# Kernel optimization log

Measured on AMD Instinct MI355X. Metric: run time of the kernel, lower is better.

Reference implementation:

```python
import jax, jax.numpy as jnp
import numpy as np

D = 128
NH = 8
L = 3
DFF = 2048
DEPOT_IDX = 0
LN_EPS = 1e-5


def _ln(x, g, b):
    m = jnp.mean(x, -1, keepdims=True)
    v = jnp.mean((x - m) ** 2, -1, keepdims=True)
    return (x - m) / jnp.sqrt(v + LN_EPS) * g + b


def _mha(x, wqkv, bqkv, wo, bo):
    # torch nn.MultiheadAttention, batch_first, no dropout (eval)
    b, n, d = x.shape
    hd = d // NH
    qkv = x @ wqkv.T + bqkv                       # [b,n,3d]
    q, k, v = jnp.split(qkv, 3, axis=-1)
    sh = lambda t: t.reshape(b, n, NH, hd).transpose(0, 2, 1, 3)
    q, k, v = sh(q), sh(k), sh(v)
    att = jax.nn.softmax(jnp.einsum('bhqd,bhkd->bhqk', q, k) * (hd ** -0.5), axis=-1)
    o = jnp.einsum('bhqk,bhkd->bhqd', att, v).transpose(0, 2, 1, 3).reshape(b, n, d)
    return o @ wo.T + bo


def _encoder(c, w_inp, b_inp, wqkv, bqkv, wo, bo, w1, b1, w2, b2, g1, be1, g2, be2):
    h = c @ w_inp.T + b_inp                       # [b,n,d]

    def layer(h, p):
        (wqkv, bqkv, wo, bo, w1, b1, w2, b2, g1, be1, g2, be2) = p
        # post-LN TransformerEncoderLayer (torch default norm_first=False, relu)
        h = _ln(h + _mha(h, wqkv, bqkv, wo, bo), g1, be1)
        ff = jax.nn.relu(h @ w1.T + b1) @ w2.T + b2
        h = _ln(h + ff, g2, be2)
        return h, None

    h, _ = jax.lax.scan(layer, h, (wqkv, bqkv, wo, bo, w1, b1, w2, b2, g1, be1, g2, be2))
    return h


def _greedy(c, start_node, params):
    (w_inp, b_inp, wqkv, bqkv, wo, bo, w1, b1, w2, b2, g1, be1, g2, be2,
     wq, bq, wk, bk) = params
    b, n, _ = c.shape
    e = _encoder(c, w_inp, b_inp, wqkv, bqkv, wo, bo, w1, b1, w2, b2, g1, be1, g2, be2)
    kproj = e @ wk.T + bk                          # [b,n,d], hoisted (loop-invariant)
    scale = D ** (-0.5)
    neg = jnp.finfo(e.dtype).min
    bidx = jnp.arange(b)

    vis0 = jnp.zeros((b, n), bool).at[:, DEPOT_IDX].set(True)

    def step(carry, _):
        node, vis = carry
        mask = vis.at[bidx, node].set(True)
        q = e[bidx, node] @ wq.T + bq              # [b,d]
        logits = jnp.einsum('bd,bnd->bn', q, kproj) * scale
        logits = jnp.where(mask, neg, logits)
        nxt = jnp.argmax(logits, axis=-1)
        return (nxt, mask), (node, logits)

    (_, _), (tour, logits) = jax.lax.scan(step, (start_node, vis0), None, length=n - 1)
    return tour.T, logits.transpose(1, 0, 2)      # [b,n-1], [b,n-1,n]


def setup_inputs() -> dict:
    key = jax.random.key(0)
    ks = jax.random.split(key, 24)
    B, N = 512, 100
    w = lambda k, s: jax.random.normal(k, s, jnp.float32) * 0.05
    inp = {
        'c': jax.random.uniform(ks[0], (B, N, 2), jnp.float32),
        'start_node': jax.random.randint(ks[1], (B,), 1, N),
        'w_inp': w(ks[2], (D, 2)), 'b_inp': jnp.zeros((D,), jnp.float32),
        'wqkv': w(ks[3], (L, 3 * D, D)), 'bqkv': jnp.zeros((L, 3 * D), jnp.float32),
        'wo': w(ks[4], (L, D, D)), 'bo': jnp.zeros((L, D), jnp.float32),
        'w1': w(ks[5], (L, DFF, D)), 'b1': jnp.zeros((L, DFF), jnp.float32),
        'w2': w(ks[6], (L, D, DFF)), 'b2': jnp.zeros((L, D), jnp.float32),
        'g1': jnp.ones((L, D), jnp.float32), 'be1': jnp.zeros((L, D), jnp.float32),
        'g2': jnp.ones((L, D), jnp.float32), 'be2': jnp.zeros((L, D), jnp.float32),
        'wq': w(ks[7], (D, D)), 'bq': jnp.zeros((D,), jnp.float32),
        'wk': w(ks[8], (D, D)), 'bk': jnp.zeros((D,), jnp.float32),
    }
    return inp


def reference(c, start_node, w_inp, b_inp, wqkv, bqkv, wo, bo, w1, b1, w2, b2,
              g1, be1, g2, be2, wq, bq, wk, bk):
    params = (w_inp, b_inp, wqkv, bqkv, wo, bo, w1, b1, w2, b2,
              g1, be1, g2, be2, wq, bq, wk, bk)
    tour, logits = _greedy(c, start_node, params)
    return tour, logits
```

## Files before the change

kernel.cpp:

```cpp
#include <hip/hip_runtime.h>
#include <hip/hip_bf16.h>
#include <math.h>

#define D 128
#define NH 8
#define HD 16
#define NL 3
#define DFF 2048
#define NNODE 100
#define BATCH 512
#define M_TOT (BATCH * NNODE)
#define LN_EPS 1e-5f
#define NEGW (-3.0e+38f)

typedef __attribute__((ext_vector_type(8))) short bf16x8;
typedef __attribute__((ext_vector_type(4))) float f32x4;
typedef __attribute__((ext_vector_type(8))) unsigned short u16x8;

__device__ __forceinline__ unsigned short f2bf(float x) {
  unsigned u = __float_as_uint(x);
  u = u + 0x7FFFu + ((u >> 16) & 1u);
  return (unsigned short)(u >> 16);
}
__device__ __forceinline__ float bf2f(unsigned short s) {
  return __uint_as_float(((unsigned)s) << 16);
}

__global__ __launch_bounds__(256) void k_split(
    const float* __restrict__ src, unsigned short* __restrict__ hi,
    unsigned short* __restrict__ lo, int n) {
  int i = blockIdx.x * 256 + threadIdx.x;
  if (i >= n) return;
  float x = src[i];
  unsigned short h = f2bf(x);
  hi[i] = h;
  lo[i] = f2bf(x - bf2f(h));
}

__global__ __launch_bounds__(256) void k_inproj(
    const float* __restrict__ c, const float* __restrict__ w,
    const float* __restrict__ b, float* __restrict__ h,
    unsigned short* __restrict__ hhi, unsigned short* __restrict__ hlo) {
  int idx = blockIdx.x * 256 + threadIdx.x;
  if (idx >= M_TOT * D) return;
  int m = idx >> 7, d = idx & 127;
  float v = c[m * 2] * w[d * 2] + c[m * 2 + 1] * w[d * 2 + 1] + b[d];
  h[idx] = v;
  unsigned short t = f2bf(v);
  hhi[idx] = t;
  hlo[idx] = f2bf(v - bf2f(t));
}

__global__ __launch_bounds__(256) void k_gemm3(
    const unsigned short* __restrict__ Ah, const unsigned short* __restrict__ Al,
    const unsigned short* __restrict__ Wh, const unsigned short* __restrict__ Wl,
    const float* __restrict__ bias,
    float* __restrict__ C, unsigned short* __restrict__ Chi,
    unsigned short* __restrict__ Clo, int M, int N, int K, int relu_split) {
  __shared__ unsigned short sAh[64 * 40], sAl[64 * 40];
  __shared__ unsigned short sWh[128 * 40], sWl[128 * 40];
  const int m0 = blockIdx.x * 64, n0 = blockIdx.y * 128;
  const int tid = threadIdx.x, lane = tid & 63, wid = tid >> 6;
  const int wr = wid >> 1, wc = wid & 1;
  const int lr = lane & 15, lg = lane >> 4;
  f32x4 acc[2][4];
#pragma unroll
  for (int a = 0; a < 2; ++a)
#pragma unroll
    for (int b = 0; b < 4; ++b) acc[a][b] = (f32x4){0.f, 0.f, 0.f, 0.f};
  const int ar = tid >> 2, ak = (tid & 3) * 8;
  const int wrr = tid >> 1, wkk = (tid & 1) * 16;
  const bool a_ok = (m0 + ar) < M;
  const long long a_base = (long long)(m0 + ar) * K + ak;
  const long long w_base = (long long)(n0 + wrr) * K + wkk;
  for (int k0 = 0; k0 < K; k0 += 32) {
    u16x8 vah = {0, 0, 0, 0, 0, 0, 0, 0}, val = {0, 0, 0, 0, 0, 0, 0, 0};
    if (a_ok) {
      vah = *(const u16x8*)(Ah + a_base + k0);
      val = *(const u16x8*)(Al + a_base + k0);
    }
    u16x8 vwh0 = *(const u16x8*)(Wh + w_base + k0);
    u16x8 vwh1 = *(const u16x8*)(Wh + w_base + k0 + 8);
    u16x8 vwl0 = *(const u16x8*)(Wl + w_base + k0);
    u16x8 vwl1 = *(const u16x8*)(Wl + w_base + k0 + 8);
    __syncthreads();
    *(u16x8*)&sAh[ar * 40 + ak] = vah;
    *(u16x8*)&sAl[ar * 40 + ak] = val;
    *(u16x8*)&sWh[wrr * 40 + wkk] = vwh0;
    *(u16x8*)&sWh[wrr * 40 + wkk + 8] = vwh1;
    *(u16x8*)&sWl[wrr * 40 + wkk] = vwl0;
    *(u16x8*)&sWl[wrr * 40 + wkk + 8] = vwl1;
    __syncthreads();
    bf16x8 fah[2], fal[2], fwh[4], fwl[4];
#pragma unroll
    for (int fm = 0; fm < 2; ++fm) {
      int o = (wr * 32 + fm * 16 + lr) * 40 + lg * 8;
      fah[fm] = *(const bf16x8*)&sAh[o];
      fal[fm] = *(const bf16x8*)&sAl[o];
    }
#pragma unroll
    for (int fn = 0; fn < 4; ++fn) {
      int o = (wc * 64 + fn * 16 + lr) * 40 + lg * 8;
      fwh[fn] = *(const bf16x8*)&sWh[o];
      fwl[fn] = *(const bf16x8*)&sWl[o];
    }
#pragma unroll
    for (int fm = 0; fm < 2; ++fm)
#pragma unroll
      for (int fn = 0; fn < 4; ++fn) {
        acc[fm][fn] = __builtin_amdgcn_mfma_f32_16x16x32_bf16(
            fah[fm], fwl[fn], acc[fm][fn], 0, 0, 0);
        acc[fm][fn] = __builtin_amdgcn_mfma_f32_16x16x32_bf16(
            fal[fm], fwh[fn], acc[fm][fn], 0, 0, 0);
        acc[fm][fn] = __builtin_amdgcn_mfma_f32_16x16x32_bf16(
            fah[fm], fwh[fn], acc[fm][fn], 0, 0, 0);
      }
  }
#pragma unroll
  for (int fm = 0; fm < 2; ++fm) {
    int rb = m0 + wr * 32 + fm * 16 + lg * 4;
#pragma unroll
    for (int fn = 0; fn < 4; ++fn) {
      int col = n0 + wc * 64 + fn * 16 + lr;
      float bv = bias[col];
#pragma unroll
      for (int j = 0; j < 4; ++j) {
        int row = rb + j;
        if (row < M) {
          float v = acc[fm][fn][j] + bv;
          if (relu_split) {
            v = fmaxf(v, 0.f);
            unsigned short hv = f2bf(v);
            long long o = (long long)row * N + col;
            Chi[o] = hv;
            Clo[o] = f2bf(v - bf2f(hv));
          } else {
            C[(long long)row * N + col] = v;
          }
        }
      }
    }
  }
}

__global__ __launch_bounds__(256) void k_gemm(
    const float* __restrict__ A, long long sA,
    const float* __restrict__ W, long long sW,
    const float* __restrict__ bias,
    float* __restrict__ C, long long sC,
    int M, int N, int K, float scale, int relu) {
  __shared__ float As[32][72];
  __shared__ float Ws[32][72];
  A += (long long)blockIdx.z * sA;
  W += (long long)blockIdx.z * sW;
  C += (long long)blockIdx.z * sC;
  int m0 = blockIdx.x * 64, n0 = blockIdx.y * 64;
  int tid = threadIdx.x;
  int lx = tid & 31, ly = tid >> 5;
  int tc = tid & 15, tr = tid >> 4;
  float acc[4][4] = {};
  for (int k0 = 0; k0 < K; k0 += 32) {
#pragma unroll
    for (int i = 0; i < 8; ++i) {
      int m = m0 + ly + i * 8;
      As[lx][ly + i * 8] = (m < M) ? A[(long long)m * K + k0 + lx] : 0.f;
      int n = n0 + ly + i * 8;
      Ws[lx][ly + i * 8] = (n < N) ? W[(long long)n * K + k0 + lx] : 0.f;
    }
    __syncthreads();
#pragma unroll
    for (int k = 0; k < 32; ++k) {
      float4 av = *(const float4*)&As[k][tr * 4];
      float4 wv = *(const float4*)&Ws[k][tc * 4];
      const float* ap = (const float*)&av;
      const float* wp = (const float*)&wv;
#pragma unroll
      for (int i = 0; i < 4; ++i)
#pragma unroll
        for (int j = 0; j < 4; ++j)
          acc[i][j] = fmaf(ap[i], wp[j], acc[i][j]);
    }
    __syncthreads();
  }
#pragma unroll
  for (int i = 0; i < 4; ++i) {
    int m = m0 + tr * 4 + i;
    if (m >= M) continue;
#pragma unroll
    for (int j = 0; j < 4; ++j) {
      int n = n0 + tc * 4 + j;
      if (n >= N) continue;
      float v = acc[i][j] * scale;
      if (bias) v += bias[n];
      if (relu) v = fmaxf(v, 0.f);
      C[(long long)m * N + n] = v;
    }
  }
}

__global__ __launch_bounds__(256) void k_attn(
    const float* __restrict__ qkv, unsigned short* __restrict__ aoh,
    unsigned short* __restrict__ aol) {
  __shared__ float Qs[NNODE][20];
  __shared__ float Ks[NNODE][20];
  __shared__ float Vs[NNODE][20];
  __shared__ float Ss[NNODE][101];
  int bh = blockIdx.x;
  int b = bh >> 3, hh = bh & 7;
  const float* base = qkv + (long long)b * NNODE * 384 + hh * HD;
  int tid = threadIdx.x;
  for (int idx = tid; idx < NNODE * HD; idx += 256) {
    int n = idx >> 4, d2 = idx & 15;
    Qs[n][d2] = base[(long long)n * 384 + d2];
    Ks[n][d2] = base[(long long)n * 384 + 128 + d2];
    Vs[n][d2] = base[(long long)n * 384 + 256 + d2];
  }
  __syncthreads();
  for (int p = tid; p < NNODE * NNODE; p += 256) {
    int i = p / 100, j = p - i * 100;
    const float4* qv = (const float4*)&Qs[i][0];
    const float4* kv = (const float4*)&Ks[j][0];
    float s = 0.f;
#pragma unroll
    for (int t = 0; t < 4; ++t) {
      float4 q = qv[t], k = kv[t];
      s = fmaf(q.x, k.x, s);
      s = fmaf(q.y, k.y, s);
      s = fmaf(q.z, k.z, s);
      s = fmaf(q.w, k.w, s);
    }
    Ss[i][j] = s * 0.25f;
  }
  __syncthreads();
  if (tid < NNODE) {
    float mx = -INFINITY;
    for (int j = 0; j < NNODE; ++j) mx = fmaxf(mx, Ss[tid][j]);
    float sum = 0.f;
    for (int j = 0; j < NNODE; ++j) {
      float e = expf(Ss[tid][j] - mx);
      Ss[tid][j] = e;
      sum += e;
    }
    for (int j = 0; j < NNODE; ++j) Ss[tid][j] = Ss[tid][j] / sum;
  }
  __syncthreads();
  for (int p = tid; p < NNODE * HD; p += 256) {
    int i = p >> 4, d2 = p & 15;
    float o = 0.f;
    for (int k = 0; k < NNODE; ++k) o = fmaf(Ss[i][k], Vs[k][d2], o);
    long long idx = ((long long)b * NNODE + i) * D + hh * HD + d2;
    unsigned short hv = f2bf(o);
    aoh[idx] = hv;
    aol[idx] = f2bf(o - bf2f(hv));
  }
}

__global__ __launch_bounds__(256) void k_ln(
    float* __restrict__ h, const float* __restrict__ add,
    const float* __restrict__ g, const float* __restrict__ be,
    unsigned short* __restrict__ hhi, unsigned short* __restrict__ hlo) {
  int row = blockIdx.x * 4 + (threadIdx.x >> 6);
  int lane = threadIdx.x & 63;
  float2 hv = ((const float2*)(h + (long long)row * D))[lane];
  float2 av = ((const float2*)(add + (long long)row * D))[lane];
  float x0 = hv.x + av.x, x1 = hv.y + av.y;
  float s = x0 + x1;
  for (int off = 32; off; off >>= 1) s += __shfl_xor(s, off);
  float mean = s * (1.f / 128.f);
  float d0 = x0 - mean, d1 = x1 - mean;
  float v = d0 * d0 + d1 * d1;
  for (int off = 32; off; off >>= 1) v += __shfl_xor(v, off);
  float sd = sqrtf(v * (1.f / 128.f) + LN_EPS);
  float2 gv = ((const float2*)g)[lane], bv = ((const float2*)be)[lane];
  float o0 = d0 / sd * gv.x + bv.x;
  float o1 = d1 / sd * gv.y + bv.y;
  long long ix = (long long)row * D + lane * 2;
  h[ix] = o0;
  h[ix + 1] = o1;
  unsigned short t0 = f2bf(o0), t1 = f2bf(o1);
  hhi[ix] = t0;
  hlo[ix] = f2bf(o0 - bf2f(t0));
  hhi[ix + 1] = t1;
  hlo[ix + 1] = f2bf(o1 - bf2f(t1));
}

__global__ __launch_bounds__(64) void k_decode(
    const float* __restrict__ S, const int* __restrict__ start,
    float* __restrict__ tour, float* __restrict__ logits) {
  __shared__ float Sl[NNODE * NNODE];
  int b = blockIdx.x;
  const float* Sg = S + (long long)b * NNODE * NNODE;
  int l = threadIdx.x;
  for (int i = l; i < NNODE * NNODE; i += 64) Sl[i] = Sg[i];
  __syncthreads();
  unsigned long long visLo = 1ull, visHi = 0ull;
  int node = start[b];
  float* lg = logits + (long long)b * 99 * 100;
  for (int t = 0; t < 99; ++t) {
    if (node < 64) visLo |= 1ull << node;
    else visHi |= 1ull << (node - 64);
    const float* row = &Sl[node * 100];
    float c0 = ((visLo >> l) & 1ull) ? NEGW : row[l];
    float c1 = NEGW;
    int j2 = l + 64;
    if (j2 < NNODE && !((visHi >> l) & 1ull)) c1 = row[j2];
    lg[t * 100 + l] = c0;
    if (j2 < NNODE) lg[t * 100 + j2] = c1;
    if (l == 0) tour[b * 99 + t] = (float)node;
    float v = c0;
    int idx = l;
    if (c1 > v) { v = c1; idx = j2; }
    for (int off = 32; off; off >>= 1) {
      float ov = __shfl_xor(v, off);
      int oi = __shfl_xor(idx, off);
      if (ov > v || (ov == v && oi < idx)) { v = ov; idx = oi; }
    }
    node = idx;
  }
}

extern "C" void kernel_launch(void* const* d_in, const int* in_sizes, int n_in,
                              void* d_out, int out_size, void* d_ws, size_t ws_size,
                              hipStream_t stream) {
  const float* c     = (const float*)d_in[0];
  const int*   start = (const int*)d_in[1];
  const float* w_inp = (const float*)d_in[2];
  const float* b_inp = (const float*)d_in[3];
  const float* wqkv  = (const float*)d_in[4];
  const float* bqkv  = (const float*)d_in[5];
  const float* wo    = (const float*)d_in[6];
  const float* bo    = (const float*)d_in[7];
  const float* w1    = (const float*)d_in[8];
  const float* b1    = (const float*)d_in[9];
  const float* w2    = (const float*)d_in[10];
  const float* b2    = (const float*)d_in[11];
  const float* g1    = (const float*)d_in[12];
  const float* be1   = (const float*)d_in[13];
  const float* g2    = (const float*)d_in[14];
  const float* be2   = (const float*)d_in[15];
  const float* wq    = (const float*)d_in[16];
  const float* bq    = (const float*)d_in[17];
  const float* wk    = (const float*)d_in[18];
  const float* bk    = (const float*)d_in[19];

  float* h = (float*)d_ws;
  unsigned short* h_hi = (unsigned short*)((char*)d_ws + 26214400);
  unsigned short* h_lo = h_hi + (size_t)M_TOT * D;
  unsigned short* wsp  = (unsigned short*)((char*)d_ws + 52428800);
  unsigned short* wqkvh = wsp;
  unsigned short* wqkvl = wsp + 147456;
  unsigned short* woh   = wsp + 294912;
  unsigned short* wol   = wsp + 344064;
  unsigned short* w1h   = wsp + 393216;
  unsigned short* w1l   = wsp + 1179648;
  unsigned short* w2h   = wsp + 1966080;
  unsigned short* w2l   = wsp + 2752512;
  unsigned short* wqh   = wsp + 3538944;
  unsigned short* wql   = wsp + 3555328;
  unsigned short* wkh   = wsp + 3571712;
  unsigned short* wkl   = wsp + 3588096;
  float* wsArena = (float*)((char*)d_ws + 59637760);
  long long R = (long long)ws_size - 59637760LL;
  if (R < 0) R = 0;

  float* tour   = (float*)d_out;
  float* logits = (float*)d_out + (size_t)BATCH * (NNODE - 1);
  long long LBYTES = (long long)BATCH * (NNODE - 1) * NNODE * 4;

  float* encArena = (R >= LBYTES) ? wsArena : logits;
  long long E = (R >= LBYTES) ? R : LBYTES;

  long long CB = E / 256000;
  if (CB < 1) CB = 1;
  if (CB > BATCH) CB = BATCH;
  long long RB = (E / 8704) & ~3LL;
  if (RB < 4) RB = 4;
  if (RB > M_TOT) RB = M_TOT;
  long long CB2 = R / 142400;
  if (CB2 < 1) CB2 = 1;
  if (CB2 > BATCH) CB2 = BATCH;

  k_split<<<576, 256, 0, stream>>>(wqkv, wqkvh, wqkvl, 147456);
  k_split<<<192, 256, 0, stream>>>(wo, woh, wol, 49152);
  k_split<<<3072, 256, 0, stream>>>(w1, w1h, w1l, 786432);
  k_split<<<3072, 256, 0, stream>>>(w2, w2h, w2l, 786432);
  k_split<<<64, 256, 0, stream>>>(wq, wqh, wql, 16384);
  k_split<<<64, 256, 0, stream>>>(wk, wkh, wkl, 16384);

  k_inproj<<<(M_TOT * D + 255) / 256, 256, 0, stream>>>(c, w_inp, b_inp, h,
                                                        h_hi, h_lo);

  for (int l = 0; l < NL; ++l) {
    unsigned short* wqkvh_l = wqkvh + (size_t)l * 49152;
    unsigned short* wqkvl_l = wqkvl + (size_t)l * 49152;
    unsigned short* woh_l = woh + (size_t)l * 16384;
    unsigned short* wol_l = wol + (size_t)l * 16384;
    unsigned short* w1h_l = w1h + (size_t)l * 262144;
    unsigned short* w1l_l = w1l + (size_t)l * 262144;
    unsigned short* w2h_l = w2h + (size_t)l * 262144;
    unsigned short* w2l_l = w2l + (size_t)l * 262144;
    const float* bqkv_l = bqkv + (size_t)l * 384;
    const float* bo_l = bo + (size_t)l * D;
    const float* b1_l = b1 + (size_t)l * DFF;
    const float* b2_l = b2 + (size_t)l * D;
    const float* g1_l = g1 + (size_t)l * D;
    const float* be1_l = be1 + (size_t)l * D;
    const float* g2_l = g2 + (size_t)l * D;
    const float* be2_l = be2 + (size_t)l * D;

    for (long long b0 = 0; b0 < BATCH; b0 += CB) {
      long long cb = (BATCH - b0 < CB) ? (BATCH - b0) : CB;
      long long rows = cb * NNODE;
      float* qkvbuf = encArena;
      unsigned short* aoh = (unsigned short*)(qkvbuf + rows * 384);
      unsigned short* aol = aoh + rows * D;
      float* woout = (float*)(aol + rows * D);
      float* hrow = h + b0 * NNODE * D;
      unsigned short* hhir = h_hi + b0 * NNODE * D;
      unsigned short* hlor = h_lo + b0 * NNODE * D;
      k_gemm3<<<dim3((unsigned)((rows + 63) / 64), 3), 256, 0, stream>>>(
          hhir, hlor, wqkvh_l, wqkvl_l, bqkv_l, qkvbuf, nullptr, nullptr,
          (int)rows, 384, D, 0);
      k_attn<<<(unsigned)(cb * NH), 256, 0, stream>>>(qkvbuf, aoh, aol);
      k_gemm3<<<dim3((unsigned)((rows + 63) / 64), 1), 256, 0, stream>>>(
          aoh, aol, woh_l, wol_l, bo_l, woout, nullptr, nullptr,
          (int)rows, D, D, 0);
      k_ln<<<(unsigned)(rows / 4), 256, 0, stream>>>(hrow, woout, g1_l, be1_l,
                                                     hhir, hlor);
    }

    for (long long r0 = 0; r0 < M_TOT; r0 += RB) {
      long long mr = (M_TOT - r0 < RB) ? (M_TOT - r0) : RB;
      unsigned short* ff1h = (unsigned short*)encArena;
      unsigned short* ff1l = ff1h + mr * DFF;
      float* x2 = (float*)(ff1l + mr * DFF);
      float* hrow = h + r0 * D;
      unsigned short* hhir = h_hi + r0 * D;
      unsigned short* hlor = h_lo + r0 * D;
      k_gemm3<<<dim3((unsigned)((mr + 63) / 64), DFF / 128), 256, 0, stream>>>(
          hhir, hlor, w1h_l, w1l_l, b1_l, nullptr, ff1h, ff1l,
          (int)mr, DFF, D, 1);
      k_gemm3<<<dim3((unsigned)((mr + 63) / 64), 1), 256, 0, stream>>>(
          ff1h, ff1l, w2h_l, w2l_l, b2_l, x2, nullptr, nullptr,
          (int)mr, D, DFF, 0);
      k_ln<<<(unsigned)(mr / 4), 256, 0, stream>>>(hrow, x2, g2_l, be2_l,
                                                   hhir, hlor);
    }
  }

  for (long long b0 = 0; b0 < BATCH; b0 += CB2) {
    long long cb = (BATCH - b0 < CB2) ? (BATCH - b0) : CB2;
    long long rows = cb * NNODE;
    float* qp = wsArena;
    float* kp = qp + rows * D;
    float* Sb = kp + rows * D;
    unsigned short* hhir = h_hi + b0 * NNODE * D;
    unsigned short* hlor = h_lo + b0 * NNODE * D;
    k_gemm3<<<dim3((unsigned)((rows + 63) / 64), 1), 256, 0, stream>>>(
        hhir, hlor, wqh, wql, bq, qp, nullptr, nullptr, (int)rows, D, D, 0);
    k_gemm3<<<dim3((unsigned)((rows + 63) / 64), 1), 256, 0, stream>>>(
        hhir, hlor, wkh, wkl, bk, kp, nullptr, nullptr, (int)rows, D, D, 0);
    k_gemm<<<dim3(2, 2, (unsigned)cb), 256, 0, stream>>>(
        qp, (long long)NNODE * D, kp, (long long)NNODE * D, nullptr,
        Sb, (long long)NNODE * NNODE, NNODE, NNODE, D,
        0.08838834764831845f, 0);
    k_decode<<<(unsigned)cb, 64, 0, stream>>>(Sb, start + b0, tour + b0 * 99,
                                              logits + b0 * 99 * 100);
  }
}
```

Measured before the change: 2.401 ms.

## Fuse output-projection GEMMs with residual add and LayerNorm; parallelize attention softmax

Adds a k_gemm3_ln kernel that runs the N=128 split-bf16 MFMA GEMM (Wo and FF2) and applies bias, residual add and LayerNorm in the epilogue. Row statistics are reduced across waves through shared memory. This removes the separate k_ln launches and the round trip of the fp32 intermediate buffer through global memory. The attention softmax now uses 200 threads (two per row) instead of 100, and the chunk-size divisors change because the intermediate buffer is no longer needed. The fused kernel does strided scalar stores of h, hi and lo and uncoalesced residual loads, which could cost some of the saved traffic.

```diff
diff --git a/kernel.cpp b/kernel.cpp
--- a/kernel.cpp
+++ b/kernel.cpp
@@ -141,6 +141,141 @@
       }
     }
   }
+}
+
+__global__ __launch_bounds__(256) void k_gemm3_ln(
+    const unsigned short* __restrict__ Ah, const unsigned short* __restrict__ Al,
+    const unsigned short* __restrict__ Wh, const unsigned short* __restrict__ Wl,
+    const float* __restrict__ bias, const float* __restrict__ g,
+    const float* __restrict__ be, float* __restrict__ hres,
+    unsigned short* __restrict__ hhi, unsigned short* __restrict__ hlo,
+    int M, int K) {
+  __shared__ unsigned short sAh[64 * 40], sAl[64 * 40];
+  __shared__ unsigned short sWh[128 * 40], sWl[128 * 40];
+  __shared__ float redS[64][2];
+  __shared__ float redQ[64][2];
+  const int m0 = blockIdx.x * 64;
+  const int tid = threadIdx.x, lane = tid & 63, wid = tid >> 6;
+  const int wr = wid >> 1, wc = wid & 1;
+  const int lr = lane & 15, lg = lane >> 4;
+  f32x4 acc[2][4];
+#pragma unroll
+  for (int a = 0; a < 2; ++a)
+#pragma unroll
+    for (int b = 0; b < 4; ++b) acc[a][b] = (f32x4){0.f, 0.f, 0.f, 0.f};
+  const int ar = tid >> 2, ak = (tid & 3) * 8;
+  const int wrr = tid >> 1, wkk = (tid & 1) * 16;
+  const bool a_ok = (m0 + ar) < M;
+  const long long a_base = (long long)(m0 + ar) * K + ak;
+  const long long w_base = (long long)wrr * K + wkk;
+  for (int k0 = 0; k0 < K; k0 += 32) {
+    u16x8 vah = {0, 0, 0, 0, 0, 0, 0, 0}, val = {0, 0, 0, 0, 0, 0, 0, 0};
+    if (a_ok) {
+      vah = *(const u16x8*)(Ah + a_base + k0);
+      val = *(const u16x8*)(Al + a_base + k0);
+    }
+    u16x8 vwh0 = *(const u16x8*)(Wh + w_base + k0);
+    u16x8 vwh1 = *(const u16x8*)(Wh + w_base + k0 + 8);
+    u16x8 vwl0 = *(const u16x8*)(Wl + w_base + k0);
+    u16x8 vwl1 = *(const u16x8*)(Wl + w_base + k0 + 8);
+    __syncthreads();
+    *(u16x8*)&sAh[ar * 40 + ak] = vah;
+    *(u16x8*)&sAl[ar * 40 + ak] = val;
+    *(u16x8*)&sWh[wrr * 40 + wkk] = vwh0;
+    *(u16x8*)&sWh[wrr * 40 + wkk + 8] = vwh1;
+    *(u16x8*)&sWl[wrr * 40 + wkk] = vwl0;
+    *(u16x8*)&sWl[wrr * 40 + wkk + 8] = vwl1;
+    __syncthreads();
+    bf16x8 fah[2], fal[2], fwh[4], fwl[4];
+#pragma unroll
+    for (int fm = 0; fm < 2; ++fm) {
+      int o = (wr * 32 + fm * 16 + lr) * 40 + lg * 8;
+      fah[fm] = *(const bf16x8*)&sAh[o];
+      fal[fm] = *(const bf16x8*)&sAl[o];
+    }
+#pragma unroll
+    for (int fn = 0; fn < 4; ++fn) {
+      int o = (wc * 64 + fn * 16 + lr) * 40 + lg * 8;
+      fwh[fn] = *(const bf16x8*)&sWh[o];
+      fwl[fn] = *(const bf16x8*)&sWl[o];
+    }
+#pragma unroll
+    for (int fm = 0; fm < 2; ++fm)
+#pragma unroll
+      for (int fn = 0; fn < 4; ++fn) {
+        acc[fm][fn] = __builtin_amdgcn_mfma_f32_16x16x32_bf16(
+            fah[fm], fwl[fn], acc[fm][fn], 0, 0, 0);
+        acc[fm][fn] = __builtin_amdgcn_mfma_f32_16x16x32_bf16(
+            fal[fm], fwh[fn], acc[fm][fn], 0, 0, 0);
+        acc[fm][fn] = __builtin_amdgcn_mfma_f32_16x16x32_bf16(
+            fah[fm], fwh[fn], acc[fm][fn], 0, 0, 0);
+      }
+  }
+  float x[2][4][4];
+#pragma unroll
+  for (int fm = 0; fm < 2; ++fm)
+#pragma unroll
+    for (int fn = 0; fn < 4; ++fn) {
+      int col = wc * 64 + fn * 16 + lr;
+      float bv = bias[col];
+#pragma unroll
+      for (int j = 0; j < 4; ++j) {
+        int row = m0 + wr * 32 + fm * 16 + lg * 4 + j;
+        float r = (row < M) ? hres[(long long)row * D + col] : 0.f;
+        x[fm][fn][j] = acc[fm][fn][j] + bv + r;
+      }
+    }
+#pragma unroll
+  for (int fm = 0; fm < 2; ++fm)
+#pragma unroll
+    for (int j = 0; j < 4; ++j) {
+      float s = x[fm][0][j] + x[fm][1][j] + x[fm][2][j] + x[fm][3][j];
+      s += __shfl_xor(s, 1);
+      s += __shfl_xor(s, 2);
+      s += __shfl_xor(s, 4);
+      s += __shfl_xor(s, 8);
+      if (lr == 0) redS[wr * 32 + fm * 16 + lg * 4 + j][wc] = s;
+    }
+  __syncthreads();
+  float mean[2][4];
+#pragma unroll
+  for (int fm = 0; fm < 2; ++fm)
+#pragma unroll
+    for (int j = 0; j < 4; ++j) {
+      int rl = wr * 32 + fm * 16 + lg * 4 + j;
+      mean[fm][j] = (redS[rl][0] + redS[rl][1]) * (1.f / 128.f);
+      float d0 = x[fm][0][j] - mean[fm][j];
+      float d1 = x[fm][1][j] - mean[fm][j];
+      float d2 = x[fm][2][j] - mean[fm][j];
+      float d3 = x[fm][3][j] - mean[fm][j];
+      float q = d0 * d0 + d1 * d1 + d2 * d2 + d3 * d3;
+      q += __shfl_xor(q, 1);
+      q += __shfl_xor(q, 2);
+      q += __shfl_xor(q, 4);
+      q += __shfl_xor(q, 8);
+      if (lr == 0) redQ[rl][wc] = q;
+    }
+  __syncthreads();
+#pragma unroll
+  for (int fm = 0; fm < 2; ++fm)
+#pragma unroll
+    for (int j = 0; j < 4; ++j) {
+      int rl = wr * 32 + fm * 16 + lg * 4 + j;
+      int row = m0 + rl;
+      if (row >= M) continue;
+      float var = (redQ[rl][0] + redQ[rl][1]) * (1.f / 128.f);
+      float sd = sqrtf(var + LN_EPS);
+#pragma unroll
+      for (int fn = 0; fn < 4; ++fn) {
+        int col = wc * 64 + fn * 16 + lr;
+        float o = (x[fm][fn][j] - mean[fm][j]) / sd * g[col] + be[col];
+        long long ix = (long long)row * D + col;
+        hres[ix] = o;
+        unsigned short t = f2bf(o);
+        hhi[ix] = t;
+        hlo[ix] = f2bf(o - bf2f(t));
+      }
+    }
 }
 
 __global__ __launch_bounds__(256) void k_gemm(
@@ -232,16 +367,29 @@
     Ss[i][j] = s * 0.25f;
   }
   __syncthreads();
-  if (tid < NNODE) {
-    float mx = -INFINITY;
-    for (int j = 0; j < NNODE; ++j) mx = fmaxf(mx, Ss[tid][j]);
+  float* red = (float*)Qs;
+  int r = tid >> 1, hf = tid & 1;
+  float* row = &Ss[r][hf * 50];
+  if (tid < 200) {
+    float mx = row[0];
+    for (int j = 1; j < 50; ++j) mx = fmaxf(mx, row[j]);
+    red[tid] = mx;
+  }
+  __syncthreads();
+  if (tid < 200) {
+    float mx = fmaxf(red[r * 2], red[r * 2 + 1]);
     float sum = 0.f;
-    for (int j = 0; j < NNODE; ++j) {
-      float e = expf(Ss[tid][j] - mx);
-      Ss[tid][j] = e;
+    for (int j = 0; j < 50; ++j) {
+      float e = expf(row[j] - mx);
+      row[j] = e;
       sum += e;
     }
-    for (int j = 0; j < NNODE; ++j) Ss[tid][j] = Ss[tid][j] / sum;
+    red[256 + tid] = sum;
+  }
+  __syncthreads();
+  if (tid < 200) {
+    float tot = red[256 + r * 2] + red[256 + r * 2 + 1];
+    for (int j = 0; j < 50; ++j) row[j] = row[j] / tot;
   }
   __syncthreads();
   for (int p = tid; p < NNODE * HD; p += 256) {
@@ -253,35 +401,6 @@
     aoh[idx] = hv;
     aol[idx] = f2bf(o - bf2f(hv));
   }
-}
-
-__global__ __launch_bounds__(256) void k_ln(
-    float* __restrict__ h, const float* __restrict__ add,
-    const float* __restrict__ g, const float* __restrict__ be,
-    unsigned short* __restrict__ hhi, unsigned short* __restrict__ hlo) {
-  int row = blockIdx.x * 4 + (threadIdx.x >> 6);
-  int lane = threadIdx.x & 63;
-  float2 hv = ((const float2*)(h + (long long)row * D))[lane];
-  float2 av = ((const float2*)(add + (long long)row * D))[lane];
-  float x0 = hv.x + av.x, x1 = hv.y + av.y;
-  float s = x0 + x1;
-  for (int off = 32; off; off >>= 1) s += __shfl_xor(s, off);
-  float mean = s * (1.f / 128.f);
-  float d0 = x0 - mean, d1 = x1 - mean;
-  float v = d0 * d0 + d1 * d1;
-  for (int off = 32; off; off >>= 1) v += __shfl_xor(v, off);
-  float sd = sqrtf(v * (1.f / 128.f) + LN_EPS);
-  float2 gv = ((const float2*)g)[lane], bv = ((const float2*)be)[lane];
-  float o0 = d0 / sd * gv.x + bv.x;
-  float o1 = d1 / sd * gv.y + bv.y;
-  long long ix = (long long)row * D + lane * 2;
-  h[ix] = o0;
-  h[ix + 1] = o1;
-  unsigned short t0 = f2bf(o0), t1 = f2bf(o1);
-  hhi[ix] = t0;
-  hlo[ix] = f2bf(o0 - bf2f(t0));
-  hhi[ix + 1] = t1;
-  hlo[ix + 1] = f2bf(o1 - bf2f(t1));
 }
 
 __global__ __launch_bounds__(64) void k_decode(
@@ -370,10 +489,10 @@
   float* encArena = (R >= LBYTES) ? wsArena : logits;
   long long E = (R >= LBYTES) ? R : LBYTES;
 
-  long long CB = E / 256000;
+  long long CB = E / 204800;
   if (CB < 1) CB = 1;
   if (CB > BATCH) CB = BATCH;
-  long long RB = (E / 8704) & ~3LL;
+  long long RB = (E / 8192) & ~3LL;
   if (RB < 4) RB = 4;
   if (RB > M_TOT) RB = M_TOT;
   long long CB2 = R / 142400;
@@ -414,7 +533,6 @@
       float* qkvbuf = encArena;
       unsigned short* aoh = (unsigned short*)(qkvbuf + rows * 384);
       unsigned short* aol = aoh + rows * D;
-      float* woout = (float*)(aol + rows * D);
       float* hrow = h + b0 * NNODE * D;
       unsigned short* hhir = h_hi + b0 * NNODE * D;
       unsigned short* hlor = h_lo + b0 * NNODE * D;
@@ -422,29 +540,24 @@
           hhir, hlor, wqkvh_l, wqkvl_l, bqkv_l, qkvbuf, nullptr, nullptr,
           (int)rows, 384, D, 0);
       k_attn<<<(unsigned)(cb * NH), 256, 0, stream>>>(qkvbuf, aoh, aol);
-      k_gemm3<<<dim3((unsigned)((rows + 63) / 64), 1), 256, 0, stream>>>(
-          aoh, aol, woh_l, wol_l, bo_l, woout, nullptr, nullptr,
-          (int)rows, D, D, 0);
-      k_ln<<<(unsigned)(rows / 4), 256, 0, stream>>>(hrow, woout, g1_l, be1_l,
-                                                     hhir, hlor);
+      k_gemm3_ln<<<(unsigned)((rows + 63) / 64), 256, 0, stream>>>(
+          aoh, aol, woh_l, wol_l, bo_l, g1_l, be1_l, hrow, hhir, hlor,
+          (int)rows, D);
     }
 
     for (long long r0 = 0; r0 < M_TOT; r0 += RB) {
       long long mr = (M_TOT - r0 < RB) ? (M_TOT - r0) : RB;
       unsigned short* ff1h = (unsigned short*)encArena;
       unsigned short* ff1l = ff1h + mr * DFF;
-      float* x2 = (float*)(ff1l + mr * DFF);
       float* hrow = h + r0 * D;
       unsigned short* hhir = h_hi + r0 * D;
       unsigned short* hlor = h_lo + r0 * D;
       k_gemm3<<<dim3((unsigned)((mr + 63) / 64), DFF / 128), 256, 0, stream>>>(
           hhir, hlor, w1h_l, w1l_l, b1_l, nullptr, ff1h, ff1l,
           (int)mr, DFF, D, 1);
-      k_gemm3<<<dim3((unsigned)((mr + 63) / 64), 1), 256, 0, stream>>>(
-          ff1h, ff1l, w2h_l, w2l_l, b2_l, x2, nullptr, nullptr,
-          (int)mr, D, DFF, 0);
-      k_ln<<<(unsigned)(mr / 4), 256, 0, stream>>>(hrow, x2, g2_l, be2_l,
-                                                   hhir, hlor);
+      k_gemm3_ln<<<(unsigned)((mr + 63) / 64), 256, 0, stream>>>(
+          ff1h, ff1l, w2h_l, w2l_l, b2_l, g2_l, be2_l, hrow, hhir, hlor,
+          (int)mr, DFF);
     }
   }
 
```

Result: faster. 2.279 ms (-5.1%).
